# Kernel tuning notes

Hardware: AMD Instinct MI355X
Metric: run time of the kernel (lower is better)

Reference implementation:

```python
import jax, jax.numpy as jnp
import numpy as np

C = 256      # in_channels
CI = 128     # inter_channels = in_channels // 2
B, H, W = 16, 64, 64
EPS = 1e-5   # BatchNorm2d default eps


def conv1x1(x, w, b=None):
    # x: (b,c,h,w), w: (o,c) -> (b,o,h,w)
    out = jnp.einsum('bchw,oc->bohw', x, w)
    if b is not None:
        out = out + b[None, :, None, None]
    return out


def maxpool2x2(x):
    b, c, h, w = x.shape
    return x.reshape(b, c, h // 2, 2, w // 2, 2).max(axis=(3, 5))


def setup_inputs() -> dict:
    key = jax.random.key(0)
    ks = jax.random.split(key, 12)
    s_in = 1.0 / np.sqrt(C)
    s_int = 1.0 / np.sqrt(CI)
    return {
        'x': jax.random.normal(ks[0], (B, C, H, W), jnp.float32),
        'y': jax.random.normal(ks[1], (B, C, H, W), jnp.float32),
        'theta_w': jax.random.uniform(ks[2], (CI, C), jnp.float32, -s_in, s_in),
        'theta_b': jax.random.uniform(ks[3], (CI,), jnp.float32, -s_in, s_in),
        'phi_w': jax.random.uniform(ks[4], (CI, C), jnp.float32, -s_in, s_in),
        'phi_b': jax.random.uniform(ks[5], (CI,), jnp.float32, -s_in, s_in),
        'g_w': jax.random.uniform(ks[6], (CI, C), jnp.float32, -s_in, s_in),
        'g_b': jax.random.uniform(ks[7], (CI,), jnp.float32, -s_in, s_in),
        'W_w': jax.random.uniform(ks[8], (C, CI), jnp.float32, -s_int, s_int),
        'W_b': jax.random.uniform(ks[9], (C,), jnp.float32, -s_int, s_int),
        'bn_gamma': jax.random.normal(ks[10], (C,), jnp.float32) * 0.1,
        'bn_beta': jax.random.normal(ks[11], (C,), jnp.float32) * 0.1,
    }


def reference(x, y, theta_w, theta_b, phi_w, phi_b, g_w, g_b, W_w, W_b, bn_gamma, bn_beta):
    b, c, h, w = x.shape
    # g branch: 1x1 conv on y + 2x2 maxpool -> (b, CI, hw/4) -> (b, hw/4, CI)
    g_y = maxpool2x2(conv1x1(y, g_w, g_b)).reshape(b, CI, -1).transpose(0, 2, 1)
    # theta branch: 1x1 conv on x -> (b, hw, CI)
    theta_x = conv1x1(x, theta_w, theta_b).reshape(b, CI, -1).transpose(0, 2, 1)
    # phi branch: 1x1 conv on y + maxpool -> (b, CI, hw/4)
    phi_y = maxpool2x2(conv1x1(y, phi_w, phi_b)).reshape(b, CI, -1)
    # attention: (b, hw, hw/4)
    f = jnp.einsum('bnc,bcm->bnm', theta_x, phi_y)
    f_div_C = jax.nn.softmax(f, axis=-1)
    # z: (b, hw, CI) -> (b, CI, h, w)
    z = jnp.einsum('bnm,bmc->bnc', f_div_C, g_y)
    z = z.transpose(0, 2, 1).reshape(b, CI, h, w)
    # W: 1x1 conv + BatchNorm2d (training-mode batch stats, biased var)
    wz = conv1x1(z, W_w, W_b)
    mean = wz.mean(axis=(0, 2, 3), keepdims=True)
    var = wz.var(axis=(0, 2, 3), keepdims=True)
    wz = (wz - mean) * jax.lax.rsqrt(var + EPS)
    wz = wz * bn_gamma[None, :, None, None] + bn_beta[None, :, None, None]
    return wz + x
```

## Files before the change

kernel.cpp:

```cpp
#include <hip/hip_runtime.h>
#include <cstdint>

#define HW 4096
#define NC 256
#define CI 128
#define NB 16
#define MP 1024

typedef __bf16 bfv8 __attribute__((ext_vector_type(8)));
typedef float f32x16 __attribute__((ext_vector_type(16)));

__device__ __forceinline__ uint32_t bfr(float x) {
    uint32_t u = __float_as_uint(x);
    return (u + 0x7fffu + ((u >> 16) & 1u)) >> 16;
}
__device__ __forceinline__ uint32_t pkbf(float a, float b) {
    return bfr(a) | (bfr(b) << 16);
}
__device__ __forceinline__ float b2f_lo(uint32_t u) { return __uint_as_float(u << 16); }
__device__ __forceinline__ float b2f_hi(uint32_t u) { return __uint_as_float(u & 0xffff0000u); }

__global__ void k_castw(const float* __restrict__ a, const float* __restrict__ b,
                        const float* __restrict__ c, const float* __restrict__ d,
                        ushort* __restrict__ dst) {
    const float* srcs[4] = {a, b, c, d};
    const float* s = srcs[blockIdx.y];
    int i = (blockIdx.x * 256 + threadIdx.x) * 8;
    float4 v0 = *(const float4*)(s + i);
    float4 v1 = *(const float4*)(s + i + 4);
    uint4 o;
    o.x = pkbf(v0.x, v0.y); o.y = pkbf(v0.z, v0.w);
    o.z = pkbf(v1.x, v1.y); o.w = pkbf(v1.z, v1.w);
    *(uint4*)(dst + (size_t)blockIdx.y * 32768 + i) = o;
}

template<int O_TILE, int NT>
__global__ __launch_bounds__(256) void k_conv_mfma(
        const float* __restrict__ in, const ushort* __restrict__ wbf,
        const float* __restrict__ bias0, const float* __restrict__ bias1,
        ushort* __restrict__ outT) {
    __shared__ ushort xs[NT * 256];
    const int t = threadIdx.x;
    constexpr int tilesPerB = 4096 / NT;
    const int b = blockIdx.x / tilesPerB;
    const int n0 = (blockIdx.x % tilesPerB) * NT;
    const float* inb = in + ((size_t)b * 256) * 4096 + n0;

    constexpr int RPP = 1024 / NT;
    const int c0 = t % RPP, q = t / RPP;
    #pragma unroll
    for (int p = 0; p < 256 / RPP; p++) {
        int c = c0 + p * RPP;
        float4 v = *(const float4*)(inb + (size_t)c * 4096 + q * 4);
        #pragma unroll
        for (int j = 0; j < 4; j++) {
            int n = q * 4 + j;
            xs[n * 256 + (c ^ ((n & 7) << 3))] = (ushort)bfr((&v.x)[j]);
        }
    }
    __syncthreads();

    const int lane = t & 63, w = t >> 6;
    const int ln = lane & 31, hi = lane >> 5;
    int ob0, nb0;
    if (O_TILE == 256) { ob0 = w * 2; nb0 = 0; }
    else               { ob0 = (w & 1) * 2; nb0 = (w >> 1) * 2; }

    f32x16 acc[2][2];
    #pragma unroll
    for (int i = 0; i < 2; i++)
        #pragma unroll
        for (int j = 0; j < 2; j++)
            #pragma unroll
            for (int k = 0; k < 16; k++) acc[i][j][k] = 0.f;

    const ushort* wr0 = wbf + (size_t)(ob0 * 32 + ln) * 256 + hi * 8;
    const ushort* wr1 = wr0 + 32 * 256;
    const int nr0 = nb0 * 32 + ln, nr1 = nr0 + 32;
    const int sw0 = (nr0 & 7) << 3, sw1 = (nr1 & 7) << 3;

    #pragma unroll 4
    for (int ks = 0; ks < 16; ks++) {
        int k = ks * 16 + hi * 8;
        bfv8 wf0 = *(const bfv8*)(wr0 + ks * 16);
        bfv8 wf1 = *(const bfv8*)(wr1 + ks * 16);
        bfv8 x0 = *(const bfv8*)&xs[nr0 * 256 + (k ^ sw0)];
        bfv8 x1 = *(const bfv8*)&xs[nr1 * 256 + (k ^ sw1)];
        acc[0][0] = __builtin_amdgcn_mfma_f32_32x32x16_bf16(wf0, x0, acc[0][0], 0, 0, 0);
        acc[0][1] = __builtin_amdgcn_mfma_f32_32x32x16_bf16(wf0, x1, acc[0][1], 0, 0, 0);
        acc[1][0] = __builtin_amdgcn_mfma_f32_32x32x16_bf16(wf1, x0, acc[1][0], 0, 0, 0);
        acc[1][1] = __builtin_amdgcn_mfma_f32_32x32x16_bf16(wf1, x1, acc[1][1], 0, 0, 0);
    }

    #pragma unroll
    for (int oi = 0; oi < 2; oi++) {
        int obb = (ob0 + oi) * 32;
        #pragma unroll
        for (int grp = 0; grp < 4; grp++) {
            int og = obb + grp * 8 + hi * 4;
            const float* bp = (O_TILE == 256 && og >= 128) ? bias1 : bias0;
            float4 bv = *(const float4*)&bp[og & 127];
            #pragma unroll
            for (int ni = 0; ni < 2; ni++) {
                int n = n0 + (nb0 + ni) * 32 + ln;
                float r0 = acc[oi][ni][grp * 4 + 0] + bv.x;
                float r1 = acc[oi][ni][grp * 4 + 1] + bv.y;
                float r2 = acc[oi][ni][grp * 4 + 2] + bv.z;
                float r3 = acc[oi][ni][grp * 4 + 3] + bv.w;
                uint2 pk;
                pk.x = pkbf(r0, r1); pk.y = pkbf(r2, r3);
                *(uint2*)&outT[((size_t)b * 4096 + n) * O_TILE + og] = pk;
            }
        }
    }
}

__global__ __launch_bounds__(256) void k_pool(const ushort* __restrict__ phig,
        ushort* __restrict__ phiT, ushort* __restrict__ gout) {
    __shared__ ushort gt[128][33];
    int b = blockIdx.x >> 5, ph = blockIdx.x & 31;
    int t = threadIdx.x;
    int c8 = (t & 31) * 8, pg = t >> 5;
    const ushort* base = phig + ((size_t)b * 4096) * 256;
    #pragma unroll
    for (int i = 0; i < 4; i++) {
        int pw = pg * 4 + i;
        int m = ph * 32 + pw;
        int n00 = 128 * ph + 2 * pw;
        uint4 a = *(const uint4*)(base + (size_t)(n00) * 256 + c8);
        uint4 bb = *(const uint4*)(base + (size_t)(n00 + 1) * 256 + c8);
        uint4 cc = *(const uint4*)(base + (size_t)(n00 + 64) * 256 + c8);
        uint4 dd = *(const uint4*)(base + (size_t)(n00 + 65) * 256 + c8);
        uint4 o;
        const uint32_t* pa = &a.x; const uint32_t* pbp = &bb.x;
        const uint32_t* pc = &cc.x; const uint32_t* pd = &dd.x;
        uint32_t* po = &o.x;
        #pragma unroll
        for (int k = 0; k < 4; k++) {
            float lo = fmaxf(fmaxf(b2f_lo(pa[k]), b2f_lo(pbp[k])), fmaxf(b2f_lo(pc[k]), b2f_lo(pd[k])));
            float hi = fmaxf(fmaxf(b2f_hi(pa[k]), b2f_hi(pbp[k])), fmaxf(b2f_hi(pc[k]), b2f_hi(pd[k])));
            po[k] = (__float_as_uint(lo) >> 16) | (__float_as_uint(hi) & 0xffff0000u);
        }
        if (c8 < 128) {
            *(uint4*)&phiT[((size_t)b * MP + m) * CI + c8] = o;
        } else {
            int c = c8 - 128;
            #pragma unroll
            for (int j = 0; j < 8; j++) {
                uint32_t word = po[j >> 1];
                gt[c + j][pw] = (j & 1) ? (ushort)(word >> 16) : (ushort)(word & 0xffffu);
            }
        }
    }
    __syncthreads();
    {
        int c = t >> 1, half = t & 1;
        ushort* grow = gout + ((size_t)b * CI + c) * MP + ph * 32 + half * 16;
        uint32_t wv[8];
        #pragma unroll
        for (int k = 0; k < 8; k++) {
            wv[k] = (uint32_t)gt[c][half * 16 + 2 * k] | ((uint32_t)gt[c][half * 16 + 2 * k + 1] << 16);
        }
        *(uint4*)grow = make_uint4(wv[0], wv[1], wv[2], wv[3]);
        *(uint4*)(grow + 8) = make_uint4(wv[4], wv[5], wv[6], wv[7]);
    }
}

__global__ __launch_bounds__(512, 2) void k_attn_mfma(
        const ushort* __restrict__ thetaT, const ushort* __restrict__ phiT,
        const ushort* __restrict__ gmat, ushort* __restrict__ zout) {
    __shared__ char lds[65536];
    const int t = threadIdx.x;
    const int w = t >> 6, lane = t & 63;
    const int nq = lane & 31, hi = lane >> 5;
    const int ngrp = w & 3, h = w >> 2;
    const int b = blockIdx.x >> 5;
    const int q0 = (blockIdx.x & 31) << 7;

    {
        int row = t >> 2, s0 = (t & 3) * 4;
        const uint4* src = (const uint4*)(thetaT + ((size_t)b * HW + q0 + row) * CI) + s0;
        uint4* dstrow = (uint4*)(lds + row * 256);
        int rsw = row & 15;
        #pragma unroll
        for (int j = 0; j < 4; j++) {
            uint4 v = src[j];
            dstrow[(s0 + j) ^ rsw] = v;
        }
    }
    __syncthreads();
    bfv8 qf[8];
    {
        int row = ngrp * 32 + nq;
        int rsw = row & 15;
        #pragma unroll
        for (int ks = 0; ks < 8; ks++) {
            qf[ks] = *(const bfv8*)(lds + row * 256 + (((ks * 2 + hi) ^ rsw) << 4));
        }
    }
    __syncthreads();

    f32x16 zacc[4];
    #pragma unroll
    for (int ct = 0; ct < 4; ct++)
        #pragma unroll
        for (int i = 0; i < 16; i++) zacc[ct][i] = 0.f;
    float run_sum = 0.f;

    const int reg_r = t >> 7, tt = t & 127;
    const int hh = reg_r >> 1, kind = reg_r & 1;

    const char* phiB = lds + h * 32768;
    const char* gB   = lds + h * 32768 + 16384;
    const int rswp = nq & 15;
    const int rswg = nq & 7;

    for (int it = 0; it < 8; it++) {
        if (kind == 0) {
            int row = tt >> 1, s0 = (tt & 1) * 8;
            const uint4* src = (const uint4*)(phiT + ((size_t)b * MP + hh * 512 + it * 64 + row) * CI) + s0;
            uint4* dstrow = (uint4*)(lds + hh * 32768 + row * 256);
            int rsw = row & 15;
            #pragma unroll
            for (int j = 0; j < 8; j++) {
                uint4 v = src[j];
                dstrow[(s0 + j) ^ rsw] = v;
            }
        } else {
            int row = tt;
            const uint4* src = (const uint4*)(gmat + ((size_t)b * CI + row) * MP + hh * 512 + it * 64);
            uint4* dstrow = (uint4*)(lds + hh * 32768 + 16384 + row * 128);
            int rsw = row & 7;
            #pragma unroll
            for (int j = 0; j < 8; j++) {
                uint4 v = src[j];
                dstrow[j ^ rsw] = v;
            }
        }
        __syncthreads();

        f32x16 sA, sB;
        #pragma unroll
        for (int i = 0; i < 16; i++) { sA[i] = 0.f; sB[i] = 0.f; }
        __builtin_amdgcn_s_setprio(1);
        #pragma unroll
        for (int ks = 0; ks < 8; ks++) {
            int slot = ks * 2 + hi;
            bfv8 a0 = *(const bfv8*)(phiB + nq * 256 + ((slot ^ rswp) << 4));
            bfv8 a1 = *(const bfv8*)(phiB + (32 + nq) * 256 + ((slot ^ rswp) << 4));
            sA = __builtin_amdgcn_mfma_f32_32x32x16_bf16(a0, qf[ks], sA, 0, 0, 0);
            sB = __builtin_amdgcn_mfma_f32_32x32x16_bf16(a1, qf[ks], sB, 0, 0, 0);
        }
        __builtin_amdgcn_s_setprio(0);

        float pA[16], pB[16];
        #pragma unroll
        for (int i = 0; i < 16; i++) { pA[i] = __expf(sA[i]); run_sum += pA[i]; }
        #pragma unroll
        for (int i = 0; i < 16; i++) { pB[i] = __expf(sB[i]); run_sum += pB[i]; }

        uint32_t wA[8], wB[8], tA[8], tB[8];
        #pragma unroll
        for (int j = 0; j < 8; j++) { wA[j] = pkbf(pA[2 * j], pA[2 * j + 1]); wB[j] = pkbf(pB[2 * j], pB[2 * j + 1]); }
        #pragma unroll
        for (int j = 0; j < 8; j++) { tA[j] = (uint32_t)__shfl_xor((int)wA[j], 32, 64); tB[j] = (uint32_t)__shfl_xor((int)wB[j], 32, 64); }
        bool lo = (hi == 0);
        union PU { uint32_t u[4]; bfv8 v; } p0A, p1A, p0B, p1B;
        p0A.u[0] = lo ? wA[0] : tA[2]; p0A.u[1] = lo ? wA[1] : tA[3];
        p0A.u[2] = lo ? tA[0] : wA[2]; p0A.u[3] = lo ? tA[1] : wA[3];
        p1A.u[0] = lo ? wA[4] : tA[6]; p1A.u[1] = lo ? wA[5] : tA[7];
        p1A.u[2] = lo ? tA[4] : wA[6]; p1A.u[3] = lo ? tA[5] : wA[7];
        p0B.u[0] = lo ? wB[0] : tB[2]; p0B.u[1] = lo ? wB[1] : tB[3];
        p0B.u[2] = lo ? tB[0] : wB[2]; p0B.u[3] = lo ? tB[1] : wB[3];
        p1B.u[0] = lo ? wB[4] : tB[6]; p1B.u[1] = lo ? wB[5] : tB[7];
        p1B.u[2] = lo ? tB[4] : wB[6]; p1B.u[3] = lo ? tB[5] : wB[7];

        __builtin_amdgcn_s_setprio(1);
        #pragma unroll
        for (int ct = 0; ct < 4; ct++) {
            const char* grow = gB + (ct * 32 + nq) * 128;
            bfv8 g0 = *(const bfv8*)(grow + (((0 * 2 + hi) ^ rswg) << 4));
            bfv8 g1 = *(const bfv8*)(grow + (((1 * 2 + hi) ^ rswg) << 4));
            bfv8 g2 = *(const bfv8*)(grow + (((2 * 2 + hi) ^ rswg) << 4));
            bfv8 g3 = *(const bfv8*)(grow + (((3 * 2 + hi) ^ rswg) << 4));
            zacc[ct] = __builtin_amdgcn_mfma_f32_32x32x16_bf16(g0, p0A.v, zacc[ct], 0, 0, 0);
            zacc[ct] = __builtin_amdgcn_mfma_f32_32x32x16_bf16(g1, p1A.v, zacc[ct], 0, 0, 0);
            zacc[ct] = __builtin_amdgcn_mfma_f32_32x32x16_bf16(g2, p0B.v, zacc[ct], 0, 0, 0);
            zacc[ct] = __builtin_amdgcn_mfma_f32_32x32x16_bf16(g3, p1B.v, zacc[ct], 0, 0, 0);
        }
        __builtin_amdgcn_s_setprio(0);
        __syncthreads();
    }

    float pair_sum = run_sum + __shfl_xor(run_sum, 32, 64);
    float* ssum = (float*)(lds + 32768);
    if (hi == 0) ssum[w * 32 + nq] = pair_sum;
    __syncthreads();
    float psum = ssum[(w ^ 4) * 32 + nq];
    float rinv = 1.f / (pair_sum + psum);

    ushort* zr = zout + ((size_t)b * HW + q0 + ngrp * 32 + nq) * CI;
    const int rswz = nq & 15;
    #pragma unroll
    for (int pass = 0; pass < 2; pass++) {
        __syncthreads();
        if (h == 1) {
            #pragma unroll
            for (int cth = 0; cth < 2; cth++) {
                int ct = pass * 2 + cth;
                #pragma unroll
                for (int grp = 0; grp < 4; grp++) {
                    int slot = cth * 8 + grp * 2 + hi;
                    float4 v;
                    v.x = zacc[ct][grp * 4 + 0];
                    v.y = zacc[ct][grp * 4 + 1];
                    v.z = zacc[ct][grp * 4 + 2];
                    v.w = zacc[ct][grp * 4 + 3];
                    *(float4*)(lds + ngrp * 8192 + nq * 256 + ((slot ^ rswz) << 4)) = v;
                }
            }
        }
        __syncthreads();
        if (h == 0) {
            #pragma unroll
            for (int cth = 0; cth < 2; cth++) {
                int ct = pass * 2 + cth;
                #pragma unroll
                for (int grp = 0; grp < 4; grp++) {
                    int slot = cth * 8 + grp * 2 + hi;
                    float4 pv = *(const float4*)(lds + ngrp * 8192 + nq * 256 + ((slot ^ rswz) << 4));
                    float v0 = (zacc[ct][grp * 4 + 0] + pv.x) * rinv;
                    float v1 = (zacc[ct][grp * 4 + 1] + pv.y) * rinv;
                    float v2 = (zacc[ct][grp * 4 + 2] + pv.z) * rinv;
                    float v3 = (zacc[ct][grp * 4 + 3] + pv.w) * rinv;
                    int c0 = ct * 32 + grp * 8 + hi * 4;
                    uint2 pk;
                    pk.x = pkbf(v0, v1);
                    pk.y = pkbf(v2, v3);
                    *(uint2*)(zr + c0) = pk;
                }
            }
        }
    }
}

__global__ __launch_bounds__(256) void k_wz_mfma(
        const ushort* __restrict__ z, const ushort* __restrict__ Wbf,
        const float* __restrict__ Wb, ushort* __restrict__ wz,
        float* __restrict__ part) {
    __shared__ ushort zs[128 * 128];
    int t = threadIdx.x;
    int mtile = blockIdx.x;
    int oh = blockIdx.y;
    int b = mtile >> 5;
    int n0 = (mtile & 31) << 7;
    const ushort* zt = z + ((size_t)b * 4096 + n0) * 128;
    #pragma unroll
    for (int it = 0; it < 8; it++) {
        int d = (it * 256 + t) * 16;
        uint4 v = *(const uint4*)((const char*)zt + d);
        int n = d >> 8;
        int widx = (n << 7) + (((d & 255) ^ ((n & 7) << 4)) >> 1);
        *(uint4*)&zs[widx] = v;
    }
    __syncthreads();
    int lane = t & 63, w = t >> 6;
    int ln = lane & 31, hi = lane >> 5;
    int wr = w >> 1, wc = w & 1;
    f32x16 acc[2][2];
    #pragma unroll
    for (int i = 0; i < 2; i++)
        #pragma unroll
        for (int j = 0; j < 2; j++)
            #pragma unroll
            for (int k = 0; k < 16; k++) acc[i][j][k] = 0.f;
    const ushort* w0 = Wbf + (size_t)(oh * 128 + wc * 64 + ln) * 128 + hi * 8;
    const ushort* w1 = w0 + 32 * 128;
    int nr0 = wr * 64 + ln, nr1 = nr0 + 32;
    int sw0 = (nr0 & 7) << 3, sw1 = (nr1 & 7) << 3;
    #pragma unroll
    for (int ks = 0; ks < 8; ks++) {
        int k = ks * 16 + hi * 8;
        bfv8 a0 = *(const bfv8*)&zs[(nr0 << 7) + (k ^ sw0)];
        bfv8 a1 = *(const bfv8*)&zs[(nr1 << 7) + (k ^ sw1)];
        bfv8 b0 = *(const bfv8*)(w0 + ks * 16);
        bfv8 b1 = *(const bfv8*)(w1 + ks * 16);
        acc[0][0] = __builtin_amdgcn_mfma_f32_32x32x16_bf16(a0, b0, acc[0][0], 0, 0, 0);
        acc[0][1] = __builtin_amdgcn_mfma_f32_32x32x16_bf16(a0, b1, acc[0][1], 0, 0, 0);
        acc[1][0] = __builtin_amdgcn_mfma_f32_32x32x16_bf16(a1, b0, acc[1][0], 0, 0, 0);
        acc[1][1] = __builtin_amdgcn_mfma_f32_32x32x16_bf16(a1, b1, acc[1][1], 0, 0, 0);
    }
    #pragma unroll
    for (int obi = 0; obi < 2; obi++) {
        int o = oh * 128 + wc * 64 + obi * 32 + ln;
        float bv = Wb[o];
        ushort* orow = wz + ((size_t)b * 256 + o) * 4096 + n0;
        float s = 0.f, qq = 0.f;
        #pragma unroll
        for (int nbi = 0; nbi < 2; nbi++) {
            #pragma unroll
            for (int grp = 0; grp < 4; grp++) {
                float vals[4];
                #pragma unroll
                for (int j = 0; j < 4; j++) {
                    float v = acc[nbi][obi][grp * 4 + j] + bv;
                    vals[j] = v;
                    s += v; qq += v * v;
                }
                int n = (wr * 2 + nbi) * 32 + grp * 8 + hi * 4;
                uint2 pk;
                pk.x = pkbf(vals[0], vals[1]);
                pk.y = pkbf(vals[2], vals[3]);
                *(uint2*)(orow + n) = pk;
            }
        }
        s += __shfl_xor(s, 32, 64);
        qq += __shfl_xor(qq, 32, 64);
        if (hi == 0) {
            float* pr = part + (size_t)(mtile * 2 + wr) * 512;
            pr[o] = s;
            pr[256 + o] = qq;
        }
    }
}

__global__ __launch_bounds__(256) void k_bnstats(const float* __restrict__ part,
        const float* __restrict__ gamma, const float* __restrict__ beta,
        float* __restrict__ ss) {
    int o = blockIdx.x, t = threadIdx.x;
    float s = 0.f, q = 0.f;
    for (int k = t; k < 1024; k += 256) {
        s += part[(size_t)k * 512 + o];
        q += part[(size_t)k * 512 + 256 + o];
    }
    #pragma unroll
    for (int d = 32; d > 0; d >>= 1) { s += __shfl_down(s, d, 64); q += __shfl_down(q, d, 64); }
    __shared__ float rs[4], rq[4];
    int wave = t >> 6, lane = t & 63;
    if (lane == 0) { rs[wave] = s; rq[wave] = q; }
    __syncthreads();
    if (t == 0) {
        float S = rs[0] + rs[1] + rs[2] + rs[3];
        float Q = rq[0] + rq[1] + rq[2] + rq[3];
        const float inv = 1.0f / 65536.0f;
        float mean = S * inv;
        float var = Q * inv - mean * mean;
        float sc = gamma[o] * rsqrtf(var + 1e-5f);
        ss[o] = sc;
        ss[NC + o] = beta[o] - mean * sc;
    }
}

__global__ void k_apply(float* __restrict__ out, const ushort* __restrict__ wz,
        const float* __restrict__ x, const float* __restrict__ ss) {
    size_t i = ((size_t)blockIdx.x * 256 + threadIdx.x) * 8;
    int o = (int)((i >> 12) & 255);
    float sc = ss[o], sh = ss[NC + o];
    uint4 wv = *(const uint4*)(wz + i);
    float4 x0 = *(const float4*)(x + i);
    float4 x1 = *(const float4*)(x + i + 4);
    float4 r0, r1;
    r0.x = b2f_lo(wv.x) * sc + sh + x0.x;
    r0.y = b2f_hi(wv.x) * sc + sh + x0.y;
    r0.z = b2f_lo(wv.y) * sc + sh + x0.z;
    r0.w = b2f_hi(wv.y) * sc + sh + x0.w;
    r1.x = b2f_lo(wv.z) * sc + sh + x1.x;
    r1.y = b2f_hi(wv.z) * sc + sh + x1.y;
    r1.z = b2f_lo(wv.w) * sc + sh + x1.z;
    r1.w = b2f_hi(wv.w) * sc + sh + x1.w;
    *(float4*)(out + i) = r0;
    *(float4*)(out + i + 4) = r1;
}

extern "C" void kernel_launch(void* const* d_in, const int* in_sizes, int n_in,
                              void* d_out, int out_size, void* d_ws, size_t ws_size,
                              hipStream_t stream) {
    const float* x       = (const float*)d_in[0];
    const float* y       = (const float*)d_in[1];
    const float* theta_w = (const float*)d_in[2];
    const float* theta_b = (const float*)d_in[3];
    const float* phi_w   = (const float*)d_in[4];
    const float* phi_b   = (const float*)d_in[5];
    const float* g_w     = (const float*)d_in[6];
    const float* g_b     = (const float*)d_in[7];
    const float* W_w     = (const float*)d_in[8];
    const float* W_b     = (const float*)d_in[9];
    const float* bn_g    = (const float*)d_in[10];
    const float* bn_b    = (const float*)d_in[11];
    float* ws  = (float*)d_ws;
    float* out = (float*)d_out;

    ushort* wbf    = (ushort*)ws;
    ushort* thetaT = (ushort*)(ws + 65536);
    ushort* wzbf   = (ushort*)(ws + 65536);
    ushort* phig   = (ushort*)(ws + 4259840);
    ushort* zbuf   = (ushort*)(ws + 8454144);
    ushort* phiT   = (ushort*)(ws + 12648448);
    ushort* gbuf   = (ushort*)(ws + 13697024);
    float*  part   = ws + 14745600;
    float*  ss     = ws + 15269888;

    k_castw<<<dim3(16, 4), 256, 0, stream>>>(theta_w, phi_w, g_w, W_w, wbf);

    k_conv_mfma<128, 128><<<NB * 32, 256, 0, stream>>>(x, wbf, theta_b, theta_b, thetaT);
    k_conv_mfma<256, 64><<<NB * 64, 256, 0, stream>>>(y, wbf + 32768, phi_b, g_b, phig);

    k_pool<<<NB * 32, 256, 0, stream>>>(phig, phiT, gbuf);

    k_attn_mfma<<<NB * 32, 512, 0, stream>>>(thetaT, phiT, gbuf, zbuf);

    k_wz_mfma<<<dim3(NB * 32, 2), 256, 0, stream>>>(zbuf, wbf + 98304, W_b, wzbf, part);
    k_bnstats<<<256, 256, 0, stream>>>(part, bn_g, bn_b, ss);
    k_apply<<<8192, 256, 0, stream>>>(out, wzbf, x, ss);
}
```

Baseline: 207.4 us.

## Fuse phi/g 1x1 conv with 2x2 maxpool into one kernel

Replaces the separate phi/g conv kernel and the pool kernel with one kernel. Each block loads two image rows of y into LDS as bf16 with a swizzle, runs the MFMA GEMM, and pools inside the block using lane shuffles and LDS before writing phiT and g. This removes the round trip of the full-resolution bf16 intermediate through global memory and one kernel launch. In exchange it uses a 64KB LDS footprint at 512 threads, which limits occupancy, and it adds extra synchronization.

```diff
diff --git a/kernel.cpp b/kernel.cpp
--- a/kernel.cpp
+++ b/kernel.cpp
@@ -115,54 +115,120 @@
     }
 }
 
-__global__ __launch_bounds__(256) void k_pool(const ushort* __restrict__ phig,
+__global__ __launch_bounds__(512) void k_convpool(
+        const float* __restrict__ in, const ushort* __restrict__ wbf,
+        const float* __restrict__ bias0, const float* __restrict__ bias1,
         ushort* __restrict__ phiT, ushort* __restrict__ gout) {
-    __shared__ ushort gt[128][33];
-    int b = blockIdx.x >> 5, ph = blockIdx.x & 31;
-    int t = threadIdx.x;
-    int c8 = (t & 31) * 8, pg = t >> 5;
-    const ushort* base = phig + ((size_t)b * 4096) * 256;
-    #pragma unroll
-    for (int i = 0; i < 4; i++) {
-        int pw = pg * 4 + i;
-        int m = ph * 32 + pw;
-        int n00 = 128 * ph + 2 * pw;
-        uint4 a = *(const uint4*)(base + (size_t)(n00) * 256 + c8);
-        uint4 bb = *(const uint4*)(base + (size_t)(n00 + 1) * 256 + c8);
-        uint4 cc = *(const uint4*)(base + (size_t)(n00 + 64) * 256 + c8);
-        uint4 dd = *(const uint4*)(base + (size_t)(n00 + 65) * 256 + c8);
-        uint4 o;
-        const uint32_t* pa = &a.x; const uint32_t* pbp = &bb.x;
-        const uint32_t* pc = &cc.x; const uint32_t* pd = &dd.x;
-        uint32_t* po = &o.x;
-        #pragma unroll
-        for (int k = 0; k < 4; k++) {
-            float lo = fmaxf(fmaxf(b2f_lo(pa[k]), b2f_lo(pbp[k])), fmaxf(b2f_lo(pc[k]), b2f_lo(pd[k])));
-            float hi = fmaxf(fmaxf(b2f_hi(pa[k]), b2f_hi(pbp[k])), fmaxf(b2f_hi(pc[k]), b2f_hi(pd[k])));
-            po[k] = (__float_as_uint(lo) >> 16) | (__float_as_uint(hi) & 0xffff0000u);
-        }
-        if (c8 < 128) {
-            *(uint4*)&phiT[((size_t)b * MP + m) * CI + c8] = o;
-        } else {
-            int c = c8 - 128;
-            #pragma unroll
-            for (int j = 0; j < 8; j++) {
-                uint32_t word = po[j >> 1];
-                gt[c + j][pw] = (j & 1) ? (ushort)(word >> 16) : (ushort)(word & 0xffffu);
-            }
-        }
-    }
-    __syncthreads();
+    __shared__ char lds[65536];
+    ushort* xs = (ushort*)lds;
+    const int t = threadIdx.x;
+    const int b = blockIdx.x >> 5;
+    const int r = blockIdx.x & 31;
+    const int n0 = r * 128;
+    const float* inb = in + ((size_t)b * 256) * 4096 + n0;
+
     {
-        int c = t >> 1, half = t & 1;
-        ushort* grow = gout + ((size_t)b * CI + c) * MP + ph * 32 + half * 16;
-        uint32_t wv[8];
-        #pragma unroll
-        for (int k = 0; k < 8; k++) {
-            wv[k] = (uint32_t)gt[c][half * 16 + 2 * k] | ((uint32_t)gt[c][half * 16 + 2 * k + 1] << 16);
-        }
-        *(uint4*)grow = make_uint4(wv[0], wv[1], wv[2], wv[3]);
-        *(uint4*)(grow + 8) = make_uint4(wv[4], wv[5], wv[6], wv[7]);
+        const int c0 = t & 7, qq = t >> 3;
+        const int ch = qq >> 5, n4 = (qq & 31) * 4;
+        #pragma unroll
+        for (int p = 0; p < 16; p++) {
+            int c = c0 + ch * 8 + p * 16;
+            float4 v = *(const float4*)(inb + (size_t)c * 4096 + n4);
+            #pragma unroll
+            for (int j = 0; j < 4; j++) {
+                int n = n4 + j;
+                xs[n * 256 + (c ^ ((n & 7) << 3))] = (ushort)bfr((&v.x)[j]);
+            }
+        }
+    }
+    __syncthreads();
+
+    const int lane = t & 63, w = t >> 6;
+    const int ln = lane & 31, hi = lane >> 5;
+    const int ob0 = (w & 3) * 2;
+    const int nb0 = (w >> 2) * 2;
+    const int lr = nb0 >> 1;
+
+    f32x16 acc[2][2];
+    #pragma unroll
+    for (int i = 0; i < 2; i++)
+        #pragma unroll
+        for (int j = 0; j < 2; j++)
+            #pragma unroll
+            for (int k = 0; k < 16; k++) acc[i][j][k] = 0.f;
+
+    const ushort* wr0 = wbf + (size_t)(ob0 * 32 + ln) * 256 + hi * 8;
+    const ushort* wr1 = wr0 + 32 * 256;
+    const int nr0 = nb0 * 32 + ln, nr1 = nr0 + 32;
+    const int sw0 = (nr0 & 7) << 3, sw1 = (nr1 & 7) << 3;
+
+    #pragma unroll 4
+    for (int ks = 0; ks < 16; ks++) {
+        int k = ks * 16 + hi * 8;
+        bfv8 wf0 = *(const bfv8*)(wr0 + ks * 16);
+        bfv8 wf1 = *(const bfv8*)(wr1 + ks * 16);
+        bfv8 x0 = *(const bfv8*)&xs[nr0 * 256 + (k ^ sw0)];
+        bfv8 x1 = *(const bfv8*)&xs[nr1 * 256 + (k ^ sw1)];
+        acc[0][0] = __builtin_amdgcn_mfma_f32_32x32x16_bf16(wf0, x0, acc[0][0], 0, 0, 0);
+        acc[0][1] = __builtin_amdgcn_mfma_f32_32x32x16_bf16(wf0, x1, acc[0][1], 0, 0, 0);
+        acc[1][0] = __builtin_amdgcn_mfma_f32_32x32x16_bf16(wf1, x0, acc[1][0], 0, 0, 0);
+        acc[1][1] = __builtin_amdgcn_mfma_f32_32x32x16_bf16(wf1, x1, acc[1][1], 0, 0, 0);
+    }
+
+    __syncthreads();
+    float* poolreg = (float*)lds + lr * 8192;
+
+    #pragma unroll
+    for (int oi = 0; oi < 2; oi++) {
+        #pragma unroll
+        for (int grp = 0; grp < 4; grp++) {
+            int og = (ob0 + oi) * 32 + grp * 8 + hi * 4;
+            const float* bp = (og >= 128) ? bias1 : bias0;
+            float4 bv = *(const float4*)&bp[og & 127];
+            #pragma unroll
+            for (int ni = 0; ni < 2; ni++) {
+                #pragma unroll
+                for (int j = 0; j < 4; j++) {
+                    float v = acc[oi][ni][grp * 4 + j] + (&bv.x)[j];
+                    float hm = fmaxf(v, __shfl_xor(v, 1, 64));
+                    if ((ln & 1) == 0) {
+                        int o = og + j;
+                        poolreg[(o << 5) + ni * 16 + (ln >> 1)] = hm;
+                    }
+                }
+            }
+        }
+    }
+    __syncthreads();
+
+    const float* p0 = (const float*)lds;
+    const float* p1 = (const float*)lds + 8192;
+    {
+        int m = t >> 4, ci8 = (t & 15) * 8;
+        uint32_t pk4[4];
+        #pragma unroll
+        for (int jp = 0; jp < 4; jp++) {
+            int o0 = ci8 + jp * 2;
+            float f0 = fmaxf(p0[(o0 << 5) + m], p1[(o0 << 5) + m]);
+            float f1 = fmaxf(p0[((o0 + 1) << 5) + m], p1[((o0 + 1) << 5) + m]);
+            pk4[jp] = pkbf(f0, f1);
+        }
+        *(uint4*)&phiT[((size_t)b * MP + r * 32 + m) * CI + ci8] =
+            make_uint4(pk4[0], pk4[1], pk4[2], pk4[3]);
+    }
+    {
+        int ci = t >> 2, mq = (t & 3) * 8;
+        int o = 128 + ci;
+        uint32_t pk4[4];
+        #pragma unroll
+        for (int jp = 0; jp < 4; jp++) {
+            int mm = mq + jp * 2;
+            float f0 = fmaxf(p0[(o << 5) + mm], p1[(o << 5) + mm]);
+            float f1 = fmaxf(p0[(o << 5) + mm + 1], p1[(o << 5) + mm + 1]);
+            pk4[jp] = pkbf(f0, f1);
+        }
+        *(uint4*)&gout[((size_t)b * CI + ci) * MP + r * 32 + mq] =
+            make_uint4(pk4[0], pk4[1], pk4[2], pk4[3]);
     }
 }
 
@@ -493,7 +559,6 @@
     ushort* wbf    = (ushort*)ws;
     ushort* thetaT = (ushort*)(ws + 65536);
     ushort* wzbf   = (ushort*)(ws + 65536);
-    ushort* phig   = (ushort*)(ws + 4259840);
     ushort* zbuf   = (ushort*)(ws + 8454144);
     ushort* phiT   = (ushort*)(ws + 12648448);
     ushort* gbuf   = (ushort*)(ws + 13697024);
@@ -503,9 +568,7 @@
     k_castw<<<dim3(16, 4), 256, 0, stream>>>(theta_w, phi_w, g_w, W_w, wbf);
 
     k_conv_mfma<128, 128><<<NB * 32, 256, 0, stream>>>(x, wbf, theta_b, theta_b, thetaT);
-    k_conv_mfma<256, 64><<<NB * 64, 256, 0, stream>>>(y, wbf + 32768, phi_b, g_b, phig);
-
-    k_pool<<<NB * 32, 256, 0, stream>>>(phig, phiT, gbuf);
+    k_convpool<<<NB * 32, 512, 0, stream>>>(y, wbf + 32768, phi_b, g_b, phiT, gbuf);
 
     k_attn_mfma<<<NB * 32, 512, 0, stream>>>(thetaT, phiT, gbuf, zbuf);
 
```

Result: faster. 197.6 us (-4.7%).
